# Performance work log

Measured on AMD Instinct MI355X. Metric: run time of the kernel, lower is better.

The kernel has to match this reference:

```python
import math
import jax, jax.numpy as jnp
import numpy as np


def _conv(x, w, b, stride, pad):
    y = jax.lax.conv_general_dilated(x, w, (stride, stride), [(pad, pad), (pad, pad)],
                                     dimension_numbers=('NCHW', 'OIHW', 'NCHW'))
    return y + b[None, :, None, None]


def _deconv(x, w, b):
    y = jax.lax.conv_transpose(x, w, (2, 2), 'SAME', dimension_numbers=('NCHW', 'HWIO', 'NCHW'))
    return y + b[None, :, None, None]


def _res_stack(h, w1, b1, w2, b2):
    for i in range(w1.shape[0]):  # small fixed num_residual_layers
        r = _conv(jax.nn.relu(h), w1[i], b1[i], 1, 1)
        r = _conv(jax.nn.relu(r), w2[i], b2[i], 1, 0)
        h = h + r
    return jax.nn.relu(h)


def _gcn_edges(x, w, b, src, dst):
    n = x.shape[0]
    xl = x @ w
    deg = 1.0 + jax.ops.segment_sum(jnp.ones_like(dst, dtype=xl.dtype), dst, num_segments=n)
    dinv = jax.lax.rsqrt(deg)
    coef = (dinv[src] * dinv[dst])[:, None]
    agg = jax.ops.segment_sum(xl[src] * coef, dst, num_segments=n)
    return agg + xl / deg[:, None] + b


def setup_inputs() -> dict:
    key = jax.random.key(0)
    ks = jax.random.split(key, 40)
    B, C, H, D, E, Hg, R, L, hid = 256, 3, 64, 256, 16, 64, 32, 2, 128
    f = H // 4
    flat = hid * f * f  # 32768

    def n(k, shape, s=0.02):
        return jax.random.normal(k, shape, jnp.float32) * s

    i = jnp.arange(B - 1)
    src = jnp.concatenate([i, i + 1])
    dst = jnp.concatenate([i + 1, i])
    inp = {
        'x': jax.random.normal(ks[0], (B, C, H, H), jnp.float32),
        'eps': jax.random.normal(ks[1], (B, D), jnp.float32),
        'edge_index': jnp.stack([src, dst]).astype(jnp.int32),
        'enc_conv1_w': n(ks[2], (hid // 2, C, 4, 4)), 'enc_conv1_b': n(ks[3], (hid // 2,)),
        'enc_conv2_w': n(ks[4], (hid, hid // 2, 4, 4)), 'enc_conv2_b': n(ks[5], (hid,)),
        'enc_conv3_w': n(ks[6], (hid, hid, 3, 3)), 'enc_conv3_b': n(ks[7], (hid,)),
        'enc_res_w1': n(ks[8], (L, R, hid, 3, 3)), 'enc_res_b1': n(ks[9], (L, R)),
        'enc_res_w2': n(ks[10], (L, hid, R, 1, 1)), 'enc_res_b2': n(ks[11], (L, hid)),
        'fc_mu_w': n(ks[12], (flat, D)), 'fc_mu_b': n(ks[13], (D,)),
        'fc_logvar_w': n(ks[14], (flat, D)), 'fc_logvar_b': n(ks[15], (D,)),
        'dec_fc_w': n(ks[16], (D, flat)), 'dec_fc_b': n(ks[17], (flat,)),
        'dec_res_w1': n(ks[18], (L, R, hid, 3, 3)), 'dec_res_b1': n(ks[19], (L, R)),
        'dec_res_w2': n(ks[20], (L, hid, R, 1, 1)), 'dec_res_b2': n(ks[21], (L, hid)),
        'dec_ct1_w': n(ks[22], (4, 4, hid, hid // 2)), 'dec_ct1_b': n(ks[23], (hid // 2,)),
        'dec_ct2_w': n(ks[24], (4, 4, hid // 2, C)), 'dec_ct2_b': n(ks[25], (C,)),
        'inst_w': n(ks[26], (2, D, D), 0.05), 'inst_b': n(ks[27], (2, D), 0.02),
        'dim_adj_logits': jax.random.normal(ks[28], (D, D), jnp.float32),
        'dim_embeddings': jax.random.normal(ks[29], (D, E), jnp.float32),
        'dg1_w': n(ks[30], (E, Hg), 0.2), 'dg1_b': n(ks[31], (Hg,), 0.02),
        'dg2_w': n(ks[32], (Hg, 1), 0.2), 'dg2_b': n(ks[33], (1,), 0.02),
    }
    return inp


def reference(x, eps, edge_index, enc_conv1_w, enc_conv1_b, enc_conv2_w, enc_conv2_b,
              enc_conv3_w, enc_conv3_b, enc_res_w1, enc_res_b1, enc_res_w2, enc_res_b2,
              fc_mu_w, fc_mu_b, fc_logvar_w, fc_logvar_b, dec_fc_w, dec_fc_b,
              dec_res_w1, dec_res_b1, dec_res_w2, dec_res_b2,
              dec_ct1_w, dec_ct1_b, dec_ct2_w, dec_ct2_b,
              inst_w, inst_b, dim_adj_logits, dim_embeddings, dg1_w, dg1_b, dg2_w, dg2_b):
    B = x.shape[0]
    D = dim_adj_logits.shape[0]
    # ---- encode ----
    h = jax.nn.relu(_conv(x, enc_conv1_w, enc_conv1_b, 2, 1))
    h = jax.nn.relu(_conv(h, enc_conv2_w, enc_conv2_b, 2, 1))
    h = _conv(h, enc_conv3_w, enc_conv3_b, 1, 1)
    h = _res_stack(h, enc_res_w1, enc_res_b1, enc_res_w2, enc_res_b2)
    flat = h.reshape(B, -1)
    mu = flat @ fc_mu_w + fc_mu_b
    logvar = flat @ fc_logvar_w + fc_logvar_b
    sigma = jnp.exp(0.5 * logvar)
    # ---- instance GNN over chain tree ----
    src, dst = edge_index[0], edge_index[1]
    v = mu
    for i in range(inst_w.shape[0]):
        v = jax.nn.relu(_gcn_edges(v, inst_w[i], inst_b[i], src, dst))
    v_inst = v
    # ---- dim GNN: thresholded dense adjacency, dense GCN (math-identical to edge-list GCNConv) ----
    eye = jnp.eye(D, dtype=x.dtype)
    logits = (dim_adj_logits + dim_adj_logits.T) * (1.0 - eye)
    mask = (jax.nn.sigmoid(logits) > 0.5).astype(x.dtype) * (1.0 - eye)
    mask = jnp.where(mask.sum() > 0, mask, 1.0 - eye)  # fallback: complete graph
    a_hat = mask + eye
    dinv = jax.lax.rsqrt(a_hat.sum(1))
    norm_adj = a_hat * dinv[:, None] * dinv[None, :]
    xd = jax.nn.relu(norm_adj @ (dim_embeddings @ dg1_w) + dg1_b)
    dim_importance = (norm_adj @ (xd @ dg2_w) + dg2_b)[:, 0]
    # ---- reparameterize + decode ----
    vv = v_inst * dim_importance[None, :]
    z = mu + sigma * (eps * vv)
    hd = (z @ dec_fc_w + dec_fc_b).reshape(B, enc_conv3_w.shape[0], x.shape[2] // 4, x.shape[3] // 4)
    hd = _res_stack(hd, dec_res_w1, dec_res_b1, dec_res_w2, dec_res_b2)
    hd = jax.nn.relu(_deconv(hd, dec_ct1_w, dec_ct1_b))
    recon = _deconv(hd, dec_ct2_w, dec_ct2_b)
    # ---- ELBO ----
    log_px_z = -jnp.sum((recon - x) ** 2)
    prior = -0.5 * jnp.sum(z ** 2 + math.log(2 * math.pi))
    entropy = 0.5 * jnp.sum(1.0 + jnp.log(sigma ** 2 + 1e-8))
    elbo = log_px_z + prior + entropy
    lv = jnp.log(sigma ** 2 + 1e-8)
    kl_per_dim = -0.5 * (1.0 + lv - mu ** 2 - jnp.exp(lv))
    num_active_dims = jnp.sum(kl_per_dim.mean(0) > 0.01)
    return recon, elbo, num_active_dims, dim_importance, v_inst
```

## Files before the change

kernel.cpp:

```cpp
#include <hip/hip_runtime.h>
#include <math.h>

#define OUT_ELBO  3145728
#define OUT_NACT  3145729
#define OUT_IMP   3145730
#define OUT_VINST 3145986

__device__ __forceinline__ float relu_(float v){ return fmaxf(v, 0.f); }

__device__ __forceinline__ unsigned short f2bf(float f){
  unsigned int u = __float_as_uint(f);
  unsigned int r = (u + 0x7FFFu + ((u>>16)&1u)) >> 16;
  return (unsigned short)r;
}

typedef __attribute__((ext_vector_type(8))) short short8;
typedef __attribute__((ext_vector_type(4))) float f32x4;

__global__ __launch_bounds__(512) void k_conv1(const float* __restrict__ in,
    const float* __restrict__ w, const float* __restrict__ bias, float* __restrict__ out){
  __shared__ float li[13068];
  __shared__ float lw[1536];
  int cohalf = blockIdx.x & 1;
  int n      = blockIdx.x >> 1;
  int co0 = cohalf*32;
  int tid = threadIdx.x;
  for (int i=tid; i<13068; i+=512) li[i] = 0.f;
  __syncthreads();
  const float* ip = in + (size_t)n*12288;
  for (int i=tid; i<12288; i+=512){
    int ci = i >> 12, rem = i & 4095;
    int yy = rem >> 6, xx = rem & 63;
    li[ci*4356 + (yy+1)*66 + xx+1] = ip[i];
  }
  for (int i=tid; i<1536; i+=512){
    int t = i >> 5, c = i & 31;
    lw[i] = w[(co0+c)*48 + t];
  }
  __syncthreads();
  int x = tid & 31, y8 = tid >> 5;
  #pragma unroll
  for (int cc=0; cc<4; cc++){
    float acc[2][8];
    #pragma unroll
    for (int q=0;q<2;q++)
      #pragma unroll
      for (int c=0;c<8;c++) acc[q][c]=0.f;
    #pragma unroll
    for (int ci=0; ci<3; ci++){
      int cb = ci*4356;
      #pragma unroll
      for (int ky=0; ky<4; ky++){
        float v[2][4];
        #pragma unroll
        for (int q=0;q<2;q++){
          int y = y8 + 16*q;
          int rb = cb + (2*y+ky)*66 + 2*x;
          v[q][0]=li[rb]; v[q][1]=li[rb+1]; v[q][2]=li[rb+2]; v[q][3]=li[rb+3];
        }
        float wv[4][8];
        #pragma unroll
        for (int kx=0;kx<4;kx++){
          int wb = ((ci*4+ky)*4+kx)*32 + cc*8;
          #pragma unroll
          for (int c=0;c<8;c++) wv[kx][c] = lw[wb+c];
        }
        #pragma unroll
        for (int q=0;q<2;q++)
          #pragma unroll
          for (int kx=0;kx<4;kx++)
            #pragma unroll
            for (int c=0;c<8;c++)
              acc[q][c] += v[q][kx]*wv[kx][c];
      }
    }
    #pragma unroll
    for (int c=0;c<8;c++){
      int co = co0 + cc*8 + c;
      float bv = bias[co];
      #pragma unroll
      for (int q=0;q<2;q++){
        int y = y8 + 16*q;
        out[(((size_t)n*64+co)*32 + y)*32 + x] = relu_(acc[q][c] + bv);
      }
    }
  }
}

__global__ __launch_bounds__(256) void k_wt2(const float* __restrict__ w,
    unsigned short* __restrict__ Wt){
  int idx = blockIdx.x*256 + threadIdx.x;
  int ci = idx & 63;
  int r = idx >> 6;
  int t = r >> 7, co = r & 127;
  Wt[idx] = f2bf(w[((co*64 + ci)<<4) + t]);
}

__global__ __launch_bounds__(256) void k_at2(const float* __restrict__ in,
    unsigned short* __restrict__ At){
  __shared__ unsigned int l[256*33];
  int n = blockIdx.x, tid = threadIdx.x;
  const float* ip = in + (size_t)n*65536;
  unsigned short* Ab = At + (size_t)n*1156*64;
  for (int c=0;c<4;c++){
    __syncthreads();
    int pxg = c*256 + tid;
    for (int j=0;j<64;j+=2){
      float a = ip[j*1024 + pxg];
      float b = ip[(j+1)*1024 + pxg];
      l[tid*33 + (j>>1)] = (unsigned int)f2bf(a) | ((unsigned int)f2bf(b)<<16);
    }
    __syncthreads();
    #pragma unroll
    for (int it=0; it<8; it++){
      int u = it*256 + tid;
      int pxl = u >> 3, seg = u & 7;
      int pxg2 = c*256 + pxl;
      int y = pxg2 >> 5, x = pxg2 & 31;
      int pp = (y+1)*34 + (x+1);
      uint4 v;
      v.x = l[pxl*33 + seg*4 + 0];
      v.y = l[pxl*33 + seg*4 + 1];
      v.z = l[pxl*33 + seg*4 + 2];
      v.w = l[pxl*33 + seg*4 + 3];
      *(uint4*)(Ab + pp*64 + seg*8) = v;
    }
  }
  uint4 z; z.x=0; z.y=0; z.z=0; z.w=0;
  for (int it=0; it<5; it++){
    int u = it*256 + tid;
    if (u >= 1056) break;
    int h = u >> 3, seg = u & 7;
    int pp;
    if (h < 34) pp = h;
    else if (h < 68) pp = 1122 + (h-34);
    else { int s = h-68; pp = (1 + (s>>1))*34 + (s&1)*33; }
    *(uint4*)(Ab + pp*64 + seg*8) = z;
  }
}

__global__ __launch_bounds__(256) void k_c2mfma(const unsigned short* __restrict__ At,
    const unsigned short* __restrict__ Wt, const float* __restrict__ bias,
    float* __restrict__ out){
  int b = blockIdx.x;
  int wsw = (b & 7)*32 + (b >> 3);
  int half = wsw & 1;
  int n    = wsw >> 1;
  int tid = threadIdx.x;
  int wid = tid >> 6, lane = tid & 63;
  int wn = wid & 1, wm = wid >> 1;
  int lrow = lane & 15, lkb = lane >> 4;
  f32x4 acc[4][4];
  #pragma unroll
  for (int i=0;i<4;i++)
    #pragma unroll
    for (int j=0;j<4;j++){ acc[i][j].x=0.f; acc[i][j].y=0.f; acc[i][j].z=0.f; acc[i][j].w=0.f; }
  const unsigned short* Ab = At + (size_t)n*1156*64;
  int mbase = half*128 + wm*64;
  #pragma unroll
  for (int t=0; t<16; t++){
    int ky = t >> 2, kx = t & 3;
    #pragma unroll
    for (int kc=0; kc<2; kc++){
      int k0 = kc*32 + lkb*8;
      short8 a[4], b2[4];
      #pragma unroll
      for (int i=0;i<4;i++){
        int m = mbase + i*16 + lrow;
        int y = m >> 4, x = m & 15;
        int pp = (2*y+ky)*34 + (2*x+kx);
        a[i] = *(const short8*)(Ab + pp*64 + k0);
      }
      #pragma unroll
      for (int j=0;j<4;j++){
        int co = wn*64 + j*16 + lrow;
        b2[j] = *(const short8*)(Wt + (t*128 + co)*64 + k0);
      }
      #pragma unroll
      for (int i=0;i<4;i++)
        #pragma unroll
        for (int j=0;j<4;j++)
          acc[i][j] = __builtin_amdgcn_mfma_f32_16x16x32_bf16(a[i], b2[j], acc[i][j], 0,0,0);
    }
  }
  #pragma unroll
  for (int j=0;j<4;j++){
    int co = wn*64 + j*16 + lrow;
    float bv = bias[co];
    #pragma unroll
    for (int i=0;i<4;i++){
      int px0 = mbase + i*16 + lkb*4;
      f32x4 v = acc[i][j];
      v.x = relu_(v.x + bv); v.y = relu_(v.y + bv);
      v.z = relu_(v.z + bv); v.w = relu_(v.w + bv);
      *(f32x4*)(out + ((size_t)n*128+co)*256 + px0) = v;
    }
  }
}

__global__ __launch_bounds__(256) void k_wt(const float* __restrict__ w,
    unsigned short* __restrict__ Wt, int Co){
  int idx = blockIdx.x*256 + threadIdx.x;
  int tot = Co*128*9;
  if (idx >= tot) return;
  int ci = idx & 127;
  int r = idx >> 7;
  int t = r / Co, co = r - t*Co;
  Wt[idx] = f2bf(w[(co*128 + ci)*9 + t]);
}

__global__ __launch_bounds__(256) void k_wt1(const float* __restrict__ w,
    unsigned short* __restrict__ Wt){
  int idx = blockIdx.x*256 + threadIdx.x;
  int ci = idx & 127;
  int r = idx >> 7;
  int t = r >> 6, co = r & 63;
  Wt[idx] = f2bf(w[t*8192 + ci*64 + co]);
}

__global__ __launch_bounds__(256) void k_at(const float* __restrict__ in,
    unsigned short* __restrict__ At, int relu){
  __shared__ unsigned int l[256*67];
  int n = blockIdx.x, tid = threadIdx.x;
  for (int j=0;j<128;j+=2){
    float a = in[(n*128+j  )*256 + tid];
    float b = in[(n*128+j+1)*256 + tid];
    if (relu){ a = relu_(a); b = relu_(b); }
    l[tid*67 + (j>>1)] = (unsigned int)f2bf(a) | ((unsigned int)f2bf(b)<<16);
  }
  __syncthreads();
  unsigned short* Ab = At + (size_t)n*324*128;
  #pragma unroll
  for (int it=0; it<16; it++){
    int u = it*256 + tid;
    int px = u >> 4, seg = u & 15;
    int y = px >> 4, x = px & 15;
    int pp = (y+1)*18 + (x+1);
    uint4 v;
    v.x = l[px*67 + seg*4 + 0];
    v.y = l[px*67 + seg*4 + 1];
    v.z = l[px*67 + seg*4 + 2];
    v.w = l[px*67 + seg*4 + 3];
    *(uint4*)(Ab + pp*128 + seg*8) = v;
  }
  uint4 z; z.x=0; z.y=0; z.z=0; z.w=0;
  for (int it=0; it<5; it++){
    int u = it*256 + tid;
    if (u >= 1088) break;
    int h = u >> 4, seg = u & 15;
    int pp;
    if (h < 18) pp = h;
    else if (h < 36) pp = 306 + (h-18);
    else { int s = h-36; pp = 18 + (s>>1)*18 + (s&1)*17; }
    *(uint4*)(Ab + pp*128 + seg*8) = z;
  }
}

template<int CO>
__global__ __launch_bounds__(512) void k_c3mfma(const unsigned short* __restrict__ At,
    const unsigned short* __restrict__ Wt, const float* __restrict__ bias,
    float* __restrict__ out){
  constexpr int WNW = (CO==128) ? 2 : 1;
  constexpr int WMW = 8/WNW;
  constexpr int MT  = 16/WMW;
  constexpr int NT  = (CO/16)/WNW;
  __shared__ short8 lA[16][324];
  int n = blockIdx.x;
  int tid = threadIdx.x;
  const short8* src = (const short8*)(At + (size_t)n*324*128);
  #pragma unroll
  for (int it=0; it<11; it++){
    int u = it*512 + tid;
    if (u < 5184) lA[u & 15][u >> 4] = src[u];
  }
  __syncthreads();
  int wid = tid >> 6, lane = tid & 63;
  int wn = wid % WNW, wm = wid / WNW;
  int lrow = lane & 15, lkb = lane >> 4;
  f32x4 acc[MT][NT];
  #pragma unroll
  for (int i=0;i<MT;i++)
    #pragma unroll
    for (int j=0;j<NT;j++){ acc[i][j].x=0.f; acc[i][j].y=0.f; acc[i][j].z=0.f; acc[i][j].w=0.f; }
  for (int t=0; t<9; t++){
    int ky = t/3, kx = t - 3*(t/3);
    #pragma unroll
    for (int kc=0; kc<4; kc++){
      int ch = kc*4 + lkb;
      int k0 = kc*32 + lkb*8;
      short8 a[MT], b[NT];
      #pragma unroll
      for (int i=0;i<MT;i++){
        int m = wm*(MT*16) + i*16 + lrow;
        int y = m >> 4, x = m & 15;
        int pp = (y+ky)*18 + (x+kx);
        a[i] = lA[ch][pp];
      }
      #pragma unroll
      for (int j=0;j<NT;j++){
        int co = wn*(NT*16) + j*16 + lrow;
        b[j] = *(const short8*)(Wt + (t*CO + co)*128 + k0);
      }
      #pragma unroll
      for (int i=0;i<MT;i++)
        #pragma unroll
        for (int j=0;j<NT;j++)
          acc[i][j] = __builtin_amdgcn_mfma_f32_16x16x32_bf16(a[i], b[j], acc[i][j], 0,0,0);
    }
  }
  #pragma unroll
  for (int j=0;j<NT;j++){
    int co = wn*(NT*16) + j*16 + lrow;
    float bv = bias[co];
    #pragma unroll
    for (int i=0;i<MT;i++){
      int px0 = wm*(MT*16) + i*16 + lkb*4;
      f32x4 v = acc[i][j];
      v.x += bv; v.y += bv; v.z += bv; v.w += bv;
      *(f32x4*)(out + ((size_t)n*CO+co)*256 + px0) = v;
    }
  }
}

__global__ __launch_bounds__(512) void k_dc1mfma(const unsigned short* __restrict__ At,
    const unsigned short* __restrict__ Wt, const float* __restrict__ bias,
    float* __restrict__ out){
  __shared__ short8 lA[16][324];
  int b = blockIdx.x;
  int wsw = (b & 7)*64 + (b >> 3);
  int half = wsw & 1;
  int n    = wsw >> 1;
  int tid = threadIdx.x;
  const short8* src = (const short8*)(At + (size_t)n*324*128);
  #pragma unroll
  for (int it=0; it<11; it++){
    int u = it*512 + tid;
    if (u < 5184) lA[u & 15][u >> 4] = src[u];
  }
  __syncthreads();
  int wid = tid >> 6, lane = tid & 63;
  int cls = half*2 + (wid >> 2);
  int wm  = wid & 3;
  int p_y = cls >> 1, p_x = cls & 1;
  int lrow = lane & 15, lkb = lane >> 4;
  f32x4 acc[4][4];
  #pragma unroll
  for (int i=0;i<4;i++)
    #pragma unroll
    for (int j=0;j<4;j++){ acc[i][j].x=0.f; acc[i][j].y=0.f; acc[i][j].z=0.f; acc[i][j].w=0.f; }
  #pragma unroll
  for (int kc=0; kc<16; kc++){
    int tapi = kc >> 2;
    int a = tapi >> 1, bb = tapi & 1;
    int ch = (kc & 3)*4 + lkb;
    int k0 = (kc & 3)*32 + lkb*8;
    int t = (p_y + 2*a)*4 + (p_x + 2*bb);
    short8 av[4], bv[4];
    #pragma unroll
    for (int i=0;i<4;i++){
      int m = wm*64 + i*16 + lrow;
      int gy = m >> 4, gx = m & 15;
      int pp = (gy + p_y + a)*18 + (gx + p_x + bb);
      av[i] = lA[ch][pp];
    }
    #pragma unroll
    for (int j=0;j<4;j++){
      int co = j*16 + lrow;
      bv[j] = *(const short8*)(Wt + (t*64 + co)*128 + k0);
    }
    #pragma unroll
    for (int i=0;i<4;i++)
      #pragma unroll
      for (int j=0;j<4;j++)
        acc[i][j] = __builtin_amdgcn_mfma_f32_16x16x32_bf16(av[i], bv[j], acc[i][j], 0,0,0);
  }
  #pragma unroll
  for (int j=0;j<4;j++){
    int co = j*16 + lrow;
    float bvf = bias[co];
    float* op = out + (((size_t)n*64 + co)*4 + cls)*256;
    #pragma unroll
    for (int i=0;i<4;i++){
      int m0 = wm*64 + i*16 + lkb*4;
      f32x4 v = acc[i][j];
      v.x = relu_(v.x + bvf); v.y = relu_(v.y + bvf);
      v.z = relu_(v.z + bvf); v.w = relu_(v.w + bvf);
      *(f32x4*)(op + m0) = v;
    }
  }
}

__global__ __launch_bounds__(256) void k_res1x1(const float* __restrict__ r,
    const float* __restrict__ w, const float* __restrict__ bias, float* __restrict__ h){
  int tid = threadIdx.x, n = blockIdx.x;
  float rv[32];
  #pragma unroll
  for (int ci=0;ci<32;ci++) rv[ci] = relu_(r[(n*32+ci)*256 + tid]);
  for (int co=0;co<128;co++){
    float a = bias[co];
    const float* wp = w + co*32;
    #pragma unroll
    for (int ci=0;ci<32;ci++) a += rv[ci]*wp[ci];
    h[(n*128+co)*256 + tid] += a;
  }
}

__global__ __launch_bounds__(256) void k_f2b(const float* __restrict__ in,
    unsigned short* __restrict__ out, int n4, int relu){
  int i = blockIdx.x*256 + threadIdx.x;
  if (i >= n4) return;
  float4 v = ((const float4*)in)[i];
  if (relu){ v.x=relu_(v.x); v.y=relu_(v.y); v.z=relu_(v.z); v.w=relu_(v.w); }
  uint2 o;
  o.x = (unsigned int)f2bf(v.x) | ((unsigned int)f2bf(v.y)<<16);
  o.y = (unsigned int)f2bf(v.z) | ((unsigned int)f2bf(v.w)<<16);
  ((uint2*)out)[i] = o;
}

__global__ __launch_bounds__(256) void k_wtd(const float* __restrict__ w,
    unsigned short* __restrict__ Wt){
  __shared__ unsigned int l[256*65];
  int j0 = blockIdx.x*256;
  int tid = threadIdx.x;
  for (int half=0; half<2; half++){
    __syncthreads();
    int kb = half*128;
    for (int k=0;k<128;k+=2){
      float a = w[(size_t)(kb+k  )*32768 + j0 + tid];
      float b = w[(size_t)(kb+k+1)*32768 + j0 + tid];
      l[tid*65 + (k>>1)] = (unsigned int)f2bf(a) | ((unsigned int)f2bf(b)<<16);
    }
    __syncthreads();
    #pragma unroll
    for (int it=0; it<16; it++){
      int u = it*256 + tid;
      int j = u >> 4, seg = u & 15;
      uint4 v;
      v.x = l[j*65 + seg*4 + 0];
      v.y = l[j*65 + seg*4 + 1];
      v.z = l[j*65 + seg*4 + 2];
      v.w = l[j*65 + seg*4 + 3];
      *(uint4*)(Wt + (size_t)(j0+j)*256 + kb + seg*8) = v;
    }
  }
}

__global__ __launch_bounds__(256) void k_wtfc(const float* __restrict__ w,
    unsigned short* __restrict__ Wt, int dbase){
  __shared__ unsigned int l[256*65];
  int k0 = blockIdx.x*256;
  int tid = threadIdx.x;
  for (int half=0; half<2; half++){
    __syncthreads();
    int kb = half*128;
    for (int k=0;k<128;k+=2){
      float a = w[(size_t)(k0+kb+k  )*256 + tid];
      float b = w[(size_t)(k0+kb+k+1)*256 + tid];
      l[tid*65 + (k>>1)] = (unsigned int)f2bf(a) | ((unsigned int)f2bf(b)<<16);
    }
    __syncthreads();
    #pragma unroll
    for (int it=0; it<16; it++){
      int u = it*256 + tid;
      int d = u >> 4, seg = u & 15;
      uint4 v;
      v.x = l[d*65 + seg*4 + 0];
      v.y = l[d*65 + seg*4 + 1];
      v.z = l[d*65 + seg*4 + 2];
      v.w = l[d*65 + seg*4 + 3];
      *(uint4*)(Wt + (size_t)(dbase+d)*32768 + k0 + kb + seg*8) = v;
    }
  }
}

__global__ __launch_bounds__(512) void k_dfmfma(const unsigned short* __restrict__ zb,
    const unsigned short* __restrict__ Wt, const float* __restrict__ bias,
    float* __restrict__ hd){
  int jbase = blockIdx.x*128;
  int tid = threadIdx.x;
  int wid = tid >> 6, lane = tid & 63;
  int wn = wid & 1, wm = wid >> 1;
  int lrow = lane & 15, lkb = lane >> 4;
  f32x4 acc[4][4];
  #pragma unroll
  for (int i=0;i<4;i++)
    #pragma unroll
    for (int j=0;j<4;j++){ acc[i][j].x=0.f; acc[i][j].y=0.f; acc[i][j].z=0.f; acc[i][j].w=0.f; }
  #pragma unroll
  for (int kc=0; kc<8; kc++){
    int k0 = kc*32 + lkb*8;
    short8 a[4], b[4];
    #pragma unroll
    for (int i=0;i<4;i++){
      int m = wm*64 + i*16 + lrow;
      a[i] = *(const short8*)(zb + m*256 + k0);
    }
    #pragma unroll
    for (int j=0;j<4;j++){
      int jj = jbase + wn*64 + j*16 + lrow;
      b[j] = *(const short8*)(Wt + (size_t)jj*256 + k0);
    }
    #pragma unroll
    for (int i=0;i<4;i++)
      #pragma unroll
      for (int j=0;j<4;j++)
        acc[i][j] = __builtin_amdgcn_mfma_f32_16x16x32_bf16(a[i], b[j], acc[i][j], 0,0,0);
  }
  #pragma unroll
  for (int j=0;j<4;j++){
    int jj = jbase + wn*64 + j*16 + lrow;
    float bv = bias[jj];
    #pragma unroll
    for (int i=0;i<4;i++){
      int m0 = wm*64 + i*16 + lkb*4;
      f32x4 v = acc[i][j];
      hd[(size_t)(m0  )*32768 + jj] = v.x + bv;
      hd[(size_t)(m0+1)*32768 + jj] = v.y + bv;
      hd[(size_t)(m0+2)*32768 + jj] = v.z + bv;
      hd[(size_t)(m0+3)*32768 + jj] = v.w + bv;
    }
  }
}

__global__ __launch_bounds__(512) void k_efmfma(const unsigned short* __restrict__ Ab,
    const unsigned short* __restrict__ Wt, float* __restrict__ P){
  int ks = blockIdx.x >> 2;
  int ng = blockIdx.x & 3;
  int kchunk = ks*512;
  int tid = threadIdx.x;
  int wid = tid >> 6, lane = tid & 63;
  int wn = wid & 1, wm = wid >> 1;
  int lrow = lane & 15, lkb = lane >> 4;
  f32x4 acc[4][4];
  #pragma unroll
  for (int i=0;i<4;i++)
    #pragma unroll
    for (int j=0;j<4;j++){ acc[i][j].x=0.f; acc[i][j].y=0.f; acc[i][j].z=0.f; acc[i][j].w=0.f; }
  #pragma unroll
  for (int kc=0; kc<16; kc++){
    int k0 = kchunk + kc*32 + lkb*8;
    short8 a[4], b[4];
    #pragma unroll
    for (int i=0;i<4;i++){
      int m = wm*64 + i*16 + lrow;
      a[i] = *(const short8*)(Ab + (size_t)m*32768 + k0);
    }
    #pragma unroll
    for (int j=0;j<4;j++){
      int n = ng*128 + wn*64 + j*16 + lrow;
      b[j] = *(const short8*)(Wt + (size_t)n*32768 + k0);
    }
    #pragma unroll
    for (int i=0;i<4;i++)
      #pragma unroll
      for (int j=0;j<4;j++)
        acc[i][j] = __builtin_amdgcn_mfma_f32_16x16x32_bf16(a[i], b[j], acc[i][j], 0,0,0);
  }
  #pragma unroll
  for (int j=0;j<4;j++){
    int n = ng*128 + wn*64 + j*16 + lrow;
    #pragma unroll
    for (int i=0;i<4;i++){
      int m0 = wm*64 + i*16 + lkb*4;
      f32x4 v = acc[i][j];
      P[((size_t)ks*256 + m0  )*512 + n] = v.x;
      P[((size_t)ks*256 + m0+1)*512 + n] = v.y;
      P[((size_t)ks*256 + m0+2)*512 + n] = v.z;
      P[((size_t)ks*256 + m0+3)*512 + n] = v.w;
    }
  }
}

__global__ __launch_bounds__(256) void k_efred(const float* __restrict__ P,
    const float* __restrict__ bmu, const float* __restrict__ blv,
    float* __restrict__ mu, float* __restrict__ lv){
  int idx = blockIdx.x*256 + threadIdx.x;
  int m = idx >> 8, d = idx & 255;
  float sm=0.f, sl=0.f;
  for (int ks=0; ks<64; ks++){
    size_t base = ((size_t)ks*256 + m)*512;
    sm += P[base + d];
    sl += P[base + 256 + d];
  }
  mu[idx] = sm + bmu[d];
  lv[idx] = sl + blv[d];
}

__global__ void k_deg(const int* __restrict__ ei, int ne, float* __restrict__ deg,
                      float* __restrict__ dinv){
  int n = threadIdx.x;
  const int* dst = ei + ne;
  int c = 1;
  for (int e=0;e<ne;e++) c += (dst[e]==n) ? 1 : 0;
  deg[n]  = (float)c;
  dinv[n] = rsqrtf((float)c);
}

__global__ __launch_bounds__(256) void k_zero(float* __restrict__ p, int n){
  int i = blockIdx.x*256 + threadIdx.x;
  if (i<n) p[i]=0.f;
}

__global__ __launch_bounds__(256) void k_gemm256(const float* __restrict__ v,
    const float* __restrict__ w, float* __restrict__ xl){
  __shared__ float vl[256];
  int n = blockIdx.x, tid = threadIdx.x;
  vl[tid] = v[(n<<8)+tid];
  __syncthreads();
  float a=0.f;
  for (int k=0;k<256;k++) a += vl[k]*w[(k<<8)+tid];
  xl[(n<<8)+tid]=a;
}

__global__ __launch_bounds__(256) void k_edge(const int* __restrict__ ei, int ne,
    const float* __restrict__ xl, const float* __restrict__ dinv, float* __restrict__ agg){
  int e = blockIdx.x, d = threadIdx.x;
  int s = ei[e], t = ei[ne+e];
  float c = dinv[s]*dinv[t];
  atomicAdd(&agg[(t<<8)+d], xl[(s<<8)+d]*c);
}

__global__ __launch_bounds__(256) void k_gcnout(const float* __restrict__ agg,
    const float* __restrict__ xl, const float* __restrict__ deg, const float* __restrict__ bias,
    float* __restrict__ vout, float* __restrict__ vout2){
  int idx = blockIdx.x*256 + threadIdx.x;
  int n = idx>>8, d = idx&255;
  float o = relu_(agg[idx] + xl[idx]/deg[n] + bias[d]);
  vout[idx]=o;
  if (vout2) vout2[idx]=o;
}

__global__ __launch_bounds__(256) void k_y1(const float* __restrict__ emb,
    const float* __restrict__ w, float* __restrict__ y1){
  int idx = blockIdx.x*256+threadIdx.x;
  int i = idx>>6, h = idx&63;
  float a=0.f;
  #pragma unroll
  for (int k=0;k<16;k++) a += emb[i*16+k]*w[k*64+h];
  y1[idx]=a;
}

__global__ __launch_bounds__(256) void k_mask(const float* __restrict__ L,
    float* __restrict__ mask, float* __restrict__ rowcnt){
  __shared__ float red[256];
  int i = blockIdx.x, j = threadIdx.x;
  float m = (i!=j && (L[(i<<8)+j] + L[(j<<8)+i] > 0.f)) ? 1.f : 0.f;
  mask[(i<<8)+j]=m;
  red[j]=m; __syncthreads();
  for (int s=128;s>0;s>>=1){ if(j<s) red[j]+=red[j+s]; __syncthreads(); }
  if (j==0) rowcnt[i]=red[0];
}

__global__ __launch_bounds__(256) void k_dimdeg(const float* __restrict__ rowcnt,
    float* __restrict__ ddinv, float* __restrict__ fbflag){
  __shared__ float red[256];
  int i = threadIdx.x;
  red[i]=rowcnt[i]; __syncthreads();
  for (int s=128;s>0;s>>=1){ if(i<s) red[i]+=red[i+s]; __syncthreads(); }
  float fb = (red[0] > 0.f) ? 0.f : 1.f;
  float degi = 1.f + (fb>0.5f ? 255.f : rowcnt[i]);
  ddinv[i] = rsqrtf(degi);
  if (i==0) fbflag[0]=fb;
}

__global__ __launch_bounds__(64) void k_xd(const float* __restrict__ mask,
    const float* __restrict__ ddinv, const float* __restrict__ y1,
    const float* __restrict__ b, const float* __restrict__ fbflag, float* __restrict__ xd){
  int i = blockIdx.x, h = threadIdx.x;
  float fb = fbflag[0];
  float dii = ddinv[i];
  float a=0.f;
  for (int j=0;j<256;j++){
    float ah = (j==i) ? 1.f : (fb>0.5f ? 1.f : mask[(i<<8)+j]);
    a += ah*dii*ddinv[j]*y1[(j<<6)+h];
  }
  xd[(i<<6)+h] = relu_(a + b[h]);
}

__global__ __launch_bounds__(256) void k_imp(const float* __restrict__ xd,
    const float* __restrict__ w2, const float* __restrict__ b2,
    const float* __restrict__ mask, const float* __restrict__ ddinv,
    const float* __restrict__ fbflag, float* __restrict__ imp, float* __restrict__ imp_out){
  __shared__ float t[256];
  int i = threadIdx.x;
  float a=0.f;
  #pragma unroll
  for (int h=0;h<64;h++) a += xd[(i<<6)+h]*w2[h];
  t[i]=a; __syncthreads();
  float fb=fbflag[0]; float dii=ddinv[i];
  float s=0.f;
  for (int j=0;j<256;j++){
    float ah = (j==i) ? 1.f : (fb>0.5f ? 1.f : mask[(i<<8)+j]);
    s += ah*dii*ddinv[j]*t[j];
  }
  float r = s + b2[0];
  imp[i]=r; imp_out[i]=r;
}

__global__ __launch_bounds__(256) void k_reparam(const float* __restrict__ mu,
    const float* __restrict__ lv, const float* __restrict__ eps,
    const float* __restrict__ v2, const float* __restrict__ imp, float* __restrict__ z){
  int idx = blockIdx.x*256+threadIdx.x;
  int d = idx&255;
  float s = expf(0.5f*lv[idx]);
  z[idx] = mu[idx] + s*(eps[idx]*(v2[idx]*imp[d]));
}

__global__ __launch_bounds__(1024) void k_deconv2(const float* __restrict__ in,
    const float* __restrict__ w, const float* __restrict__ bias, float* __restrict__ out){
  __shared__ float tile[2][8192];
  int n = blockIdx.x;
  int tid = threadIdx.x;
  int p = tid & 31, q = tid >> 5;
  bool okc0 = p >= 1, okc2 = p < 31;
  bool okr0 = q >= 1, okr2 = q < 31;
  int r = tid >> 5, c = tid & 31;
  int su = (((r&1)<<1)|(c&1))*256 + ((r>>1)<<4) + (c>>1);
  const float* ip0 = in + (size_t)n*65536;
  float acc[2][2][3];
  #pragma unroll
  for (int py=0;py<2;py++)
    #pragma unroll
    for (int px=0;px<2;px++)
      #pragma unroll
      for (int cc=0;cc<3;cc++) acc[py][px][cc]=0.f;
  float rg[8];
  #pragma unroll
  for (int t=0;t<8;t++) rg[t] = ip0[t*1024 + su];
  #pragma unroll
  for (int t=0;t<8;t++) tile[0][t*1024 + tid] = rg[t];
  __syncthreads();
  for (int s=0; s<8; s++){
    int nxt = s+1;
    if (nxt < 8){
      #pragma unroll
      for (int t=0;t<8;t++) rg[t] = ip0[(nxt*8+t)*1024 + su];
    }
    const float* tb = tile[s&1];
    #pragma unroll
    for (int cil=0; cil<8; cil++){
      int ci = s*8 + cil;
      const float* tl = tb + cil*1024;
      float tv[3][3];
      tv[0][0] = (okr0 && okc0) ? tl[(q-1)*32 + (p-1)] : 0.f;
      tv[0][1] = okr0           ? tl[(q-1)*32 +  p   ] : 0.f;
      tv[0][2] = (okr0 && okc2) ? tl[(q-1)*32 + (p+1)] : 0.f;
      tv[1][0] = okc0           ? tl[ q   *32 + (p-1)] : 0.f;
      tv[1][1] =                  tl[ q   *32 +  p   ];
      tv[1][2] = okc2           ? tl[ q   *32 + (p+1)] : 0.f;
      tv[2][0] = (okr2 && okc0) ? tl[(q+1)*32 + (p-1)] : 0.f;
      tv[2][1] = okr2           ? tl[(q+1)*32 +  p   ] : 0.f;
      tv[2][2] = (okr2 && okc2) ? tl[(q+1)*32 + (p+1)] : 0.f;
      const float* wp = w + ci*3;
      #pragma unroll
      for (int py=0;py<2;py++){
        #pragma unroll
        for (int px=0;px<2;px++){
          const float* wAA = wp + ( py   *4 + px  )*192;
          const float* wAB = wp + ( py   *4 + px+2)*192;
          const float* wBA = wp + ((py+2)*4 + px  )*192;
          const float* wBB = wp + ((py+2)*4 + px+2)*192;
          float vAA = tv[py][px],   vAB = tv[py][px+1];
          float vBA = tv[py+1][px], vBB = tv[py+1][px+1];
          #pragma unroll
          for (int cc=0;cc<3;cc++){
            acc[py][px][cc] += vAA*wAA[cc] + vAB*wAB[cc] + vBA*wBA[cc] + vBB*wBB[cc];
          }
        }
      }
    }
    if (nxt < 8){
      #pragma unroll
      for (int t=0;t<8;t++) tile[nxt&1][t*1024 + tid] = rg[t];
    }
    __syncthreads();
  }
  #pragma unroll
  for (int cc=0;cc<3;cc++){
    float bv = bias[cc];
    float2 v0; v0.x = acc[0][0][cc] + bv; v0.y = acc[0][1][cc] + bv;
    float2 v1; v1.x = acc[1][0][cc] + bv; v1.y = acc[1][1][cc] + bv;
    *(float2*)(out + (((size_t)n*3+cc)*64 + 2*q  )*64 + 2*p) = v0;
    *(float2*)(out + (((size_t)n*3+cc)*64 + 2*q+1)*64 + 2*p) = v1;
  }
}

__global__ __launch_bounds__(256) void k_sse(const float* __restrict__ recon,
    const float* __restrict__ x, float* __restrict__ part){
  __shared__ float red[256];
  int tid = threadIdx.x;
  float a=0.f;
  for (int i = blockIdx.x*256+tid; i<3145728; i += gridDim.x*256){
    float d = recon[i]-x[i]; a += d*d;
  }
  red[tid]=a; __syncthreads();
  for (int s=128;s>0;s>>=1){ if(tid<s) red[tid]+=red[tid+s]; __syncthreads(); }
  if (tid==0) part[blockIdx.x]=red[0];
}

__global__ __launch_bounds__(256) void k_stats(const float* __restrict__ mu,
    const float* __restrict__ lv, const float* __restrict__ z,
    float* __restrict__ z2part, float* __restrict__ entpart, float* __restrict__ klflag){
  __shared__ float r1[256], r2[256], r3[256];
  int d = blockIdx.x, n = threadIdx.x;
  int idx = (n<<8) + d;
  float m = mu[idx], l = lv[idx], zz = z[idx];
  float s2e = expf(l) + 1e-8f;
  float leps = logf(s2e);
  r1[n] = zz*zz;
  r2[n] = 1.f + leps;
  r3[n] = -0.5f*(1.f + leps - m*m - s2e);
  __syncthreads();
  for (int s=128;s>0;s>>=1){
    if (n<s){ r1[n]+=r1[n+s]; r2[n]+=r2[n+s]; r3[n]+=r3[n+s]; }
    __syncthreads();
  }
  if (n==0){
    z2part[d]=r1[0]; entpart[d]=r2[0];
    klflag[d] = (r3[0]*(1.f/256.f) > 0.01f) ? 1.f : 0.f;
  }
}

__global__ __launch_bounds__(256) void k_final(const float* __restrict__ ssepart,
    const float* __restrict__ z2part, const float* __restrict__ entpart,
    const float* __restrict__ klflag, float* __restrict__ out){
  __shared__ float red[256];
  int tid = threadIdx.x;
  float s=0.f;
  for (int i=tid;i<1024;i+=256) s += ssepart[i];
  red[tid]=s; __syncthreads();
  for (int st=128;st>0;st>>=1){ if(tid<st) red[tid]+=red[tid+st]; __syncthreads(); }
  float sse = red[0]; __syncthreads();
  red[tid]=z2part[tid]; __syncthreads();
  for (int st=128;st>0;st>>=1){ if(tid<st) red[tid]+=red[tid+st]; __syncthreads(); }
  float z2 = red[0]; __syncthreads();
  red[tid]=entpart[tid]; __syncthreads();
  for (int st=128;st>0;st>>=1){ if(tid<st) red[tid]+=red[tid+st]; __syncthreads(); }
  float ent = red[0]; __syncthreads();
  red[tid]=klflag[tid]; __syncthreads();
  for (int st=128;st>0;st>>=1){ if(tid<st) red[tid]+=red[tid+st]; __syncthreads(); }
  if (tid==0){
    float logpxz  = -sse;
    float prior   = -0.5f*(z2 + 65536.f*1.8378770664093453f);
    float entropy = 0.5f*ent;
    out[OUT_ELBO] = logpxz + prior + entropy;
    out[OUT_NACT] = red[0];
  }
}

extern "C" void kernel_launch(void* const* d_in, const int* in_sizes, int n_in,
                              void* d_out, int out_size, void* d_ws, size_t ws_size,
                              hipStream_t stream){
  const float* x    = (const float*)d_in[0];
  const float* eps  = (const float*)d_in[1];
  const int*   ei   = (const int*)d_in[2];
  const float* c1w  = (const float*)d_in[3];
  const float* c1b  = (const float*)d_in[4];
  const float* c2w  = (const float*)d_in[5];
  const float* c2b  = (const float*)d_in[6];
  const float* c3w  = (const float*)d_in[7];
  const float* c3b  = (const float*)d_in[8];
  const float* erw1 = (const float*)d_in[9];
  const float* erb1 = (const float*)d_in[10];
  const float* erw2 = (const float*)d_in[11];
  const float* erb2 = (const float*)d_in[12];
  const float* fmw  = (const float*)d_in[13];
  const float* fmb  = (const float*)d_in[14];
  const float* flw  = (const float*)d_in[15];
  const float* flb  = (const float*)d_in[16];
  const float* dfw  = (const float*)d_in[17];
  const float* dfb  = (const float*)d_in[18];
  const float* drw1 = (const float*)d_in[19];
  const float* drb1 = (const float*)d_in[20];
  const float* drw2 = (const float*)d_in[21];
  const float* drb2 = (const float*)d_in[22];
  const float* t1w  = (const float*)d_in[23];
  const float* t1b  = (const float*)d_in[24];
  const float* t2w  = (const float*)d_in[25];
  const float* t2b  = (const float*)d_in[26];
  const float* iw   = (const float*)d_in[27];
  const float* ib   = (const float*)d_in[28];
  const float* Lg   = (const float*)d_in[29];
  const float* emb  = (const float*)d_in[30];
  const float* g1w  = (const float*)d_in[31];
  const float* g1b  = (const float*)d_in[32];
  const float* g2w  = (const float*)d_in[33];
  const float* g2b  = (const float*)d_in[34];
  float* out = (float*)d_out;
  float* ws  = (float*)d_ws;
  int ne = in_sizes[2] / 2;

  float* A  = ws;
  float* Bb = ws + 16777216;
  float* Cc = Bb + 8388608;
  float* Rr = A;
  float* P  = A + 2097152;
  unsigned short* At = (unsigned short*)(A + 10485760);
  unsigned short* Ab = (unsigned short*)(A + 10485760);
  unsigned short* Wt = (unsigned short*)(A + 15794176);
  unsigned short* At2 = (unsigned short*)Cc;
  unsigned short* Wt2 = (unsigned short*)(Cc + 5242880);
  unsigned short* Wtd = (unsigned short*)Cc;
  unsigned short* Atd = (unsigned short*)Cc;
  unsigned short* Wt1 = (unsigned short*)(Cc + 5308416);
  unsigned short* Wtfc = (unsigned short*)Bb;
  float* S  = Cc + 8388608;
  float* mu     = S; S += 65536;
  float* lv     = S; S += 65536;
  float* v1     = S; S += 65536;
  float* v2     = S; S += 65536;
  float* xl     = S; S += 65536;
  float* agg    = S; S += 65536;
  float* zz     = S; S += 65536;
  float* mask   = S; S += 65536;
  float* y1     = S; S += 16384;
  float* xd     = S; S += 16384;
  float* zbf    = S; S += 32768;
  float* deg    = S; S += 256;
  float* dinvb  = S; S += 256;
  float* rowcnt = S; S += 256;
  float* ddinv  = S; S += 256;
  float* fbflag = S; S += 256;
  float* impv   = S; S += 256;
  float* ssep   = S; S += 1024;
  float* z2p    = S; S += 256;
  float* entp   = S; S += 256;
  float* klf    = S; S += 256;
  unsigned short* zb = (unsigned short*)zbf;

  k_conv1<<<512,512,0,stream>>>(x, c1w, c1b, A);
  k_wt2<<<512,256,0,stream>>>(c2w, Wt2);
  for (int pass=0; pass<2; pass++){
    size_t n0 = (size_t)pass*128;
    k_at2<<<128,256,0,stream>>>(A + n0*65536, At2);
    k_c2mfma<<<256,256,0,stream>>>(At2, Wt2, c2b, Bb + n0*32768);
  }
  k_wt<<<576,256,0,stream>>>(c3w, Wt, 128);
  k_at<<<256,256,0,stream>>>(Bb, At, 0);
  k_c3mfma<128><<<256,512,0,stream>>>(At, Wt, c3b, Cc);
  k_wt<<<144,256,0,stream>>>(erw1, Wt, 32);
  k_at<<<256,256,0,stream>>>(Cc, At, 1);
  k_c3mfma<32><<<256,512,0,stream>>>(At, Wt, erb1, Rr);
  k_res1x1<<<256,256,0,stream>>>(Rr, erw2, erb2, Cc);
  k_wt<<<144,256,0,stream>>>(erw1+36864, Wt, 32);
  k_at<<<256,256,0,stream>>>(Cc, At, 1);
  k_c3mfma<32><<<256,512,0,stream>>>(At, Wt, erb1+32, Rr);
  k_res1x1<<<256,256,0,stream>>>(Rr, erw2+4096, erb2+128, Cc);
  k_f2b<<<8192,256,0,stream>>>(Cc, Ab, 2097152, 1);
  k_wtfc<<<128,256,0,stream>>>(fmw, Wtfc, 0);
  k_wtfc<<<128,256,0,stream>>>(flw, Wtfc, 256);
  k_efmfma<<<256,512,0,stream>>>(Ab, Wtfc, P);
  k_efred<<<256,256,0,stream>>>(P, fmb, flb, mu, lv);

  k_deg<<<1,256,0,stream>>>(ei, ne, deg, dinvb);
  k_gemm256<<<256,256,0,stream>>>(mu, iw, xl);
  k_zero<<<256,256,0,stream>>>(agg, 65536);
  k_edge<<<ne,256,0,stream>>>(ei, ne, xl, dinvb, agg);
  k_gcnout<<<256,256,0,stream>>>(agg, xl, deg, ib, v1, nullptr);
  k_gemm256<<<256,256,0,stream>>>(v1, iw+65536, xl);
  k_zero<<<256,256,0,stream>>>(agg, 65536);
  k_edge<<<ne,256,0,stream>>>(ei, ne, xl, dinvb, agg);
  k_gcnout<<<256,256,0,stream>>>(agg, xl, deg, ib+256, v2, out + OUT_VINST);

  k_y1<<<64,256,0,stream>>>(emb, g1w, y1);
  k_mask<<<256,256,0,stream>>>(Lg, mask, rowcnt);
  k_dimdeg<<<1,256,0,stream>>>(rowcnt, ddinv, fbflag);
  k_xd<<<256,64,0,stream>>>(mask, ddinv, y1, g1b, fbflag, xd);
  k_imp<<<1,256,0,stream>>>(xd, g2w, g2b, mask, ddinv, fbflag, impv, out + OUT_IMP);

  k_reparam<<<256,256,0,stream>>>(mu, lv, eps, v2, impv, zz);
  k_f2b<<<64,256,0,stream>>>(zz, zb, 16384, 0);
  k_wtd<<<128,256,0,stream>>>(dfw, Wtd);
  k_dfmfma<<<256,512,0,stream>>>(zb, Wtd, dfb, Bb);
  k_wt<<<144,256,0,stream>>>(drw1, Wt, 32);
  k_at<<<256,256,0,stream>>>(Bb, At, 1);
  k_c3mfma<32><<<256,512,0,stream>>>(At, Wt, drb1, Rr);
  k_res1x1<<<256,256,0,stream>>>(Rr, drw2, drb2, Bb);
  k_wt<<<144,256,0,stream>>>(drw1+36864, Wt, 32);
  k_at<<<256,256,0,stream>>>(Bb, At, 1);
  k_c3mfma<32><<<256,512,0,stream>>>(At, Wt, drb1+32, Rr);
  k_res1x1<<<256,256,0,stream>>>(Rr, drw2+4096, drb2+128, Bb);
  k_wt1<<<512,256,0,stream>>>(t1w, Wt1);
  k_at<<<256,256,0,stream>>>(Bb, Atd, 1);
  k_dc1mfma<<<512,512,0,stream>>>(Atd, Wt1, t1b, A);
  k_deconv2<<<256,1024,0,stream>>>(A, t2w, t2b, out);

  k_sse<<<1024,256,0,stream>>>(out, x, ssep);
  k_stats<<<256,256,0,stream>>>(mu, lv, zz, z2p, entp, klf);
  k_final<<<1,256,0,stream>>>(ssep, z2p, entp, klf, out);
}
```

Before: 915.0 us.

## Split deconv2 into half-image blocks with halo rows and XCD-aware block swizzle

The final transposed-conv kernel now gives each image's 32x32 input to two blocks of 512 threads, each covering 16 rows plus one halo row above and below in shared memory. This doubles the grid from 256 to 512 blocks and halves per-block LDS, aiming for better occupancy and CU coverage. A block-index swizzle spreads the two halves across XCDs. The cost is redundant halo loads and extra index arithmetic per staged element.

```diff
diff --git a/kernel.cpp b/kernel.cpp
--- a/kernel.cpp
+++ b/kernel.cpp
@@ -706,17 +706,32 @@
   z[idx] = mu[idx] + s*(eps[idx]*(v2[idx]*imp[d]));
 }
 
-__global__ __launch_bounds__(1024) void k_deconv2(const float* __restrict__ in,
+__global__ __launch_bounds__(512) void k_deconv2(const float* __restrict__ in,
     const float* __restrict__ w, const float* __restrict__ bias, float* __restrict__ out){
-  __shared__ float tile[2][8192];
-  int n = blockIdx.x;
+  __shared__ float tile[2][4608];
+  int b = blockIdx.x;
+  int wsw = (b & 7)*64 + (b >> 3);
+  int h = wsw & 1;
+  int n = wsw >> 1;
   int tid = threadIdx.x;
-  int p = tid & 31, q = tid >> 5;
+  int p = tid & 31, ql = tid >> 5;
+  int q = h*16 + ql;
   bool okc0 = p >= 1, okc2 = p < 31;
-  bool okr0 = q >= 1, okr2 = q < 31;
-  int r = tid >> 5, c = tid & 31;
-  int su = (((r&1)<<1)|(c&1))*256 + ((r>>1)<<4) + (c>>1);
   const float* ip0 = in + (size_t)n*65536;
+  int su[9]; int scil[9]; bool sv[9];
+  #pragma unroll
+  for (int t=0;t<9;t++){
+    int u = t*512 + tid;
+    if (u < 4608){
+      int cil = u / 576;
+      int rem = u - cil*576;
+      int rr = rem >> 5, c = rem & 31;
+      int dr = h*16 - 1 + rr;
+      scil[t] = cil;
+      sv[t] = ((unsigned)dr < 32u);
+      su[t] = sv[t] ? ((((dr&1)<<1)|(c&1))*256 + ((dr>>1)<<4) + (c>>1)) : 0;
+    } else { scil[t] = -1; sv[t] = false; su[t] = 0; }
+  }
   float acc[2][2][3];
   #pragma unroll
   for (int py=0;py<2;py++)
@@ -724,33 +739,38 @@
     for (int px=0;px<2;px++)
       #pragma unroll
       for (int cc=0;cc<3;cc++) acc[py][px][cc]=0.f;
-  float rg[8];
-  #pragma unroll
-  for (int t=0;t<8;t++) rg[t] = ip0[t*1024 + su];
-  #pragma unroll
-  for (int t=0;t<8;t++) tile[0][t*1024 + tid] = rg[t];
+  float rg[9];
+  #pragma unroll
+  for (int t=0;t<9;t++)
+    rg[t] = (scil[t] >= 0 && sv[t]) ? ip0[scil[t]*1024 + su[t]] : 0.f;
+  #pragma unroll
+  for (int t=0;t<9;t++){
+    int u = t*512 + tid;
+    if (u < 4608) tile[0][u] = rg[t];
+  }
   __syncthreads();
   for (int s=0; s<8; s++){
     int nxt = s+1;
     if (nxt < 8){
       #pragma unroll
-      for (int t=0;t<8;t++) rg[t] = ip0[(nxt*8+t)*1024 + su];
+      for (int t=0;t<9;t++)
+        rg[t] = (scil[t] >= 0 && sv[t]) ? ip0[(nxt*8 + scil[t])*1024 + su[t]] : 0.f;
     }
     const float* tb = tile[s&1];
     #pragma unroll
     for (int cil=0; cil<8; cil++){
       int ci = s*8 + cil;
-      const float* tl = tb + cil*1024;
+      const float* tl = tb + cil*576;
       float tv[3][3];
-      tv[0][0] = (okr0 && okc0) ? tl[(q-1)*32 + (p-1)] : 0.f;
-      tv[0][1] = okr0           ? tl[(q-1)*32 +  p   ] : 0.f;
-      tv[0][2] = (okr0 && okc2) ? tl[(q-1)*32 + (p+1)] : 0.f;
-      tv[1][0] = okc0           ? tl[ q   *32 + (p-1)] : 0.f;
-      tv[1][1] =                  tl[ q   *32 +  p   ];
-      tv[1][2] = okc2           ? tl[ q   *32 + (p+1)] : 0.f;
-      tv[2][0] = (okr2 && okc0) ? tl[(q+1)*32 + (p-1)] : 0.f;
-      tv[2][1] = okr2           ? tl[(q+1)*32 +  p   ] : 0.f;
-      tv[2][2] = (okr2 && okc2) ? tl[(q+1)*32 + (p+1)] : 0.f;
+      tv[0][0] = okc0 ? tl[ ql   *32 + (p-1)] : 0.f;
+      tv[0][1] =        tl[ ql   *32 +  p   ];
+      tv[0][2] = okc2 ? tl[ ql   *32 + (p+1)] : 0.f;
+      tv[1][0] = okc0 ? tl[(ql+1)*32 + (p-1)] : 0.f;
+      tv[1][1] =        tl[(ql+1)*32 +  p   ];
+      tv[1][2] = okc2 ? tl[(ql+1)*32 + (p+1)] : 0.f;
+      tv[2][0] = okc0 ? tl[(ql+2)*32 + (p-1)] : 0.f;
+      tv[2][1] =        tl[(ql+2)*32 +  p   ];
+      tv[2][2] = okc2 ? tl[(ql+2)*32 + (p+1)] : 0.f;
       const float* wp = w + ci*3;
       #pragma unroll
       for (int py=0;py<2;py++){
@@ -771,7 +791,10 @@
     }
     if (nxt < 8){
       #pragma unroll
-      for (int t=0;t<8;t++) tile[nxt&1][t*1024 + tid] = rg[t];
+      for (int t=0;t<9;t++){
+        int u = t*512 + tid;
+        if (u < 4608) tile[nxt&1][u] = rg[t];
+      }
     }
     __syncthreads();
   }
@@ -983,7 +1006,7 @@
   k_wt1<<<512,256,0,stream>>>(t1w, Wt1);
   k_at<<<256,256,0,stream>>>(Bb, Atd, 1);
   k_dc1mfma<<<512,512,0,stream>>>(Atd, Wt1, t1b, A);
-  k_deconv2<<<256,1024,0,stream>>>(A, t2w, t2b, out);
+  k_deconv2<<<512,512,0,stream>>>(A, t2w, t2b, out);
 
   k_sse<<<1024,256,0,stream>>>(out, x, ssep);
   k_stats<<<256,256,0,stream>>>(mu, lv, zz, z2p, entp, klf);
```

New measurement: 950.7 us. 1.04x slower.
